# Kernel tuning notes

Hardware: AMD Instinct MI355X
Metric: run time of the kernel (lower is better)

The kernel has to match this reference:

```python
import jax, jax.numpy as jnp
import numpy as np
from jax import lax

CIN, COUT, K, PAD = 256, 128, 3, 1


def setup_inputs() -> dict:
    key = jax.random.key(0)
    ks = jax.random.split(key, 5)
    N, h0, w0 = 2, 64, 64
    x = jax.random.normal(ks[0], (N, CIN, h0, w0), jnp.float32)
    lateral_feat = jax.random.normal(ks[1], (N, COUT, 1, 1), jnp.float32)
    trans_w = jax.random.normal(ks[2], (CIN, COUT, K, K), jnp.float32) * 0.02
    off_w1 = jax.random.normal(ks[3], (64, COUT, 3, 3), jnp.float32) * 0.02
    off_b1 = jnp.zeros((64,), jnp.float32)
    off_w2 = jax.random.normal(ks[4], (2 * K * K, 64, 3, 3), jnp.float32) * 0.02
    off_b2 = jnp.zeros((2 * K * K,), jnp.float32)
    return dict(x=x, lateral_feat=lateral_feat, trans_w=trans_w,
                off_w1=off_w1, off_b1=off_b1, off_w2=off_w2, off_b2=off_b2)


def _conv2d(x, w, b, pad):
    y = lax.conv_general_dilated(x, w, (1, 1), [(pad, pad), (pad, pad)],
                                 dimension_numbers=('NCHW', 'OIHW', 'NCHW'))
    return y + b[None, :, None, None]


def _conv_transpose2d(x, w, stride, pad, out_pad):
    # torch ConvTranspose2d weight layout: [Cin, Cout, k, k]
    k = w.shape[2]
    wt = jnp.flip(w, (2, 3)).transpose(1, 0, 2, 3)  # [Cout, Cin, k, k]
    lo = k - 1 - pad
    hi = k - 1 - pad + out_pad
    return lax.conv_general_dilated(x, wt, (1, 1), [(lo, hi), (lo, hi)],
                                    lhs_dilation=(stride, stride),
                                    dimension_numbers=('NCHW', 'OIHW', 'NCHW'))


def _deform_conv2d(x, offset, w, pad):
    # x [N,C,H,W], offset [N,2*K*K,H,W] (y,x interleaved per kernel tap), w [O,C,K,K]
    N, C, H, W = x.shape
    O = w.shape[0]
    KK = K * K
    off = offset.reshape(N, KK, 2, H, W)
    ky = jnp.arange(KK) // K
    kx = jnp.arange(KK) % K
    py = jnp.arange(H)[None, None, :, None] + (ky - pad)[None, :, None, None] + off[:, :, 0]
    px = jnp.arange(W)[None, None, None, :] + (kx - pad)[None, :, None, None] + off[:, :, 1]
    y0 = jnp.floor(py)
    x0 = jnp.floor(px)
    dy = py - y0
    dx = px - x0
    y0i = y0.astype(jnp.int32)
    x0i = x0.astype(jnp.int32)
    xf = x.reshape(N, C, H * W)

    def corner(yi, xi, wgt):
        valid = (yi >= 0) & (yi < H) & (xi >= 0) & (xi < W)
        idx = (jnp.clip(yi, 0, H - 1) * W + jnp.clip(xi, 0, W - 1)).reshape(N, -1)
        v = jnp.take_along_axis(xf, idx[:, None, :], axis=2).reshape(N, C, KK, H, W)
        return v * (wgt * valid)[:, None]

    sampled = (corner(y0i, x0i, (1 - dy) * (1 - dx))
               + corner(y0i, x0i + 1, (1 - dy) * dx)
               + corner(y0i + 1, x0i, dy * (1 - dx))
               + corner(y0i + 1, x0i + 1, dy * dx))  # [N,C,KK,H,W]
    return jnp.einsum('nckhw,ock->nohw', sampled, w.reshape(O, C, KK))


def reference(x, lateral_feat, trans_w, off_w1, off_b1, off_w2, off_b2):
    up = _conv_transpose2d(x, trans_w, 2, PAD, 1)          # [N, COUT, 2h0, 2w0]
    h = jax.nn.relu(_conv2d(lateral_feat, off_w1, off_b1, 1))
    offset = jnp.tanh(_conv2d(h, off_w2, off_b2, 1))       # [N, 18, 1, 1]
    N, C, H, W = up.shape
    # offset.repeat(1, 1, H, W) with 1x1 spatial input == broadcast to full grid
    offset = jnp.broadcast_to(offset, (N, 2 * K * K, H, W))
    # deform_conv2d uses trans_conv weight [O=CIN, I=COUT, K, K], stride=1, pad=PAD
    return _deform_conv2d(up, offset, trans_w, PAD)        # [N, CIN, H, W]
```

## Files before the change

### kernel.cpp

```cpp
#include <hip/hip_runtime.h>
#include <hip/hip_fp16.h>
#include <math.h>

typedef __attribute__((ext_vector_type(8))) _Float16 f16x8;
typedef __attribute__((ext_vector_type(4))) float f32x4;

__device__ __forceinline__ unsigned short f2h(float f) {
    __half h = __float2half_rn(f);
    union { __half h; unsigned short u; } v; v.h = h; return v.u;
}
__device__ __forceinline__ unsigned pk2h(float lo, float hi) {
    __half2 h = __floats2half2_rn(lo, hi);
    union { __half2 h; unsigned u; } v; v.h = h; return v.u;
}

#define BARRIER() do { asm volatile("s_waitcnt lgkmcnt(0)" ::: "memory"); \
                       __builtin_amdgcn_s_barrier(); } while (0)

__device__ __forceinline__ void blend_store_h(uint4 uA, uint4 uB, uint4 uC, uint4 uD,
                                              __half2 w0, __half2 w1, __half2 w2, __half2 w3,
                                              unsigned short* dst) {
    union U { uint4 u; __half2 h[4]; };
    U a, b, c, d, r;
    a.u = uA; b.u = uB; c.u = uC; d.u = uD;
#pragma unroll
    for (int i = 0; i < 4; ++i)
        r.h[i] = __hfma2(w0, a.h[i], __hfma2(w1, b.h[i], __hfma2(w2, c.h[i], __hmul2(w3, d.h[i]))));
    *(uint4*)dst = r.u;
}

__global__ __launch_bounds__(256) void k_prep(const float* __restrict__ x,
                                              const float* __restrict__ lat,
                                              const float* __restrict__ tw,
                                              const float* __restrict__ w1,
                                              const float* __restrict__ b1,
                                              const float* __restrict__ w2,
                                              const float* __restrict__ b2,
                                              unsigned short* __restrict__ xp,
                                              unsigned short* __restrict__ A2f,
                                              unsigned short* __restrict__ Awf,
                                              unsigned short* __restrict__ upp,
                                              int* __restrict__ ipar,
                                              float* __restrict__ fpar) {
    __shared__ float sm[8420];
    int b = blockIdx.x, t = threadIdx.x;
    if (b == 0) {
        for (int i = t; i < 8192; i += 256) sm[(i >> 7) * 129 + (i & 127)] = w1[i * 9 + 4];
        __syncthreads();
        if (t < 128) {
            int n = t >> 6, o = t & 63;
            float s = b1[o];
            const float* ln = lat + n * 128;
#pragma unroll 8
            for (int c = 0; c < 128; ++c) s += ln[c] * sm[o * 129 + c];
            sm[8256 + t] = fmaxf(s, 0.f);
        }
        __syncthreads();
        if (t < 36) {
            int n = t / 18, j = t % 18;
            float s = b2[j];
            for (int o = 0; o < 64; ++o) s += sm[8256 + n * 64 + o] * w2[(j * 64 + o) * 9 + 4];
            float ov = tanhf(s);
            ov = fminf(fmaxf(ov, -0.999999f), 0.999999f);
            sm[8384 + t] = ov;
        }
        __syncthreads();
        if (t < 36) {
            int n = t / 18, j = t % 18;
            int tap = j >> 1, d = j & 1;
            float ov = sm[8384 + t];
            float fl = floorf(ov);
            int kc = d ? (tap % 3) : (tap / 3);
            ipar[(n * 9 + tap) * 2 + d] = kc - 1 + (int)fl;
            fpar[(n * 9 + tap) * 2 + d] = ov - fl;
        }
    } else if (b < 145) {
        int slot = (b - 1) * 256 + t;
        int l = slot & 63;
        int mi = (slot >> 6) & 3;
        int w = (slot >> 8) & 3;
        int k = slot >> 10;
        int row = w * 64 + mi * 16 + (l & 15);
        int kq = l >> 4;
        unsigned short v[8];
#pragma unroll
        for (int j = 0; j < 8; ++j) {
            int kcol = k * 32 + kq * 8 + j;
            int tap = kcol >> 7, c = kcol & 127;
            v[j] = f2h(tw[(row * 128 + c) * 9 + tap]);
        }
        unsigned p0 = (unsigned)v[0] | ((unsigned)v[1] << 16);
        unsigned p1 = (unsigned)v[2] | ((unsigned)v[3] << 16);
        unsigned p2 = (unsigned)v[4] | ((unsigned)v[5] << 16);
        unsigned p3 = (unsigned)v[6] | ((unsigned)v[7] << 16);
        *(uint4*)(A2f + slot * 8) = make_uint4(p0, p1, p2, p3);
    } else if (b < 289) {
        int slot = (b - 145) * 256 + t;
        int l = slot & 63;
        int mi = (slot >> 6) & 3;
        int wm = (slot >> 8) & 1;
        int k = slot >> 9;
        int row = wm * 64 + mi * 16 + (l & 15);
        int kq = l >> 4;
        unsigned short v[8];
#pragma unroll
        for (int j = 0; j < 8; ++j) {
            int kcol = k * 32 + kq * 8 + j;
            int t9 = kcol >> 8, ci = kcol & 255;
            int ky = t9 / 3, kx = t9 - ky * 3;
            v[j] = f2h(tw[(ci * 128 + row) * 9 + (2 - ky) * 3 + (2 - kx)]);
        }
        unsigned p0 = (unsigned)v[0] | ((unsigned)v[1] << 16);
        unsigned p1 = (unsigned)v[2] | ((unsigned)v[3] << 16);
        unsigned p2 = (unsigned)v[4] | ((unsigned)v[5] << 16);
        unsigned p3 = (unsigned)v[6] | ((unsigned)v[7] << 16);
        *(uint4*)(Awf + slot * 8) = make_uint4(p0, p1, p2, p3);
    } else if (b < 801) {
        int bb = b - 289;
        int h = bb & 63, cq = (bb >> 6) & 3, n = bb >> 8;
        int c0 = cq * 64;
        {
            int wcol = t & 63, sub = t >> 6;
            for (int r = 0; r < 16; ++r) {
                int ci_l = r * 4 + sub;
                sm[ci_l * 65 + wcol] = x[((n * 256 + c0 + ci_l) * 64 + h) * 64 + wcol];
            }
        }
        __syncthreads();
        int wcol = t >> 2, cg = t & 3;
        unsigned short* dst = xp + (size_t)n * (65 * 65 * 256) + (h * 65 + wcol) * 256 + c0 + cg * 16;
        unsigned pk[8];
#pragma unroll
        for (int j = 0; j < 8; ++j)
            pk[j] = pk2h(sm[(cg * 16 + 2 * j) * 65 + wcol], sm[(cg * 16 + 2 * j + 1) * 65 + wcol]);
        *(uint4*)dst = make_uint4(pk[0], pk[1], pk[2], pk[3]);
        *(uint4*)(dst + 8) = make_uint4(pk[4], pk[5], pk[6], pk[7]);
    } else {
        int g = (b - 801) * 256 + t;
        int n2 = g >= 16640 ? 1 : 0;
        int i = g - n2 * 16640;
        int px_id = i >> 4, chv = i & 15;
        int r, c;
        if (px_id < 528) {
            int rr = px_id / 132;
            r = rr < 2 ? rr : 128 + rr;
            c = px_id - rr * 132;
        } else {
            int jj = px_id - 528;
            r = 2 + (jj >> 2);
            int cc = jj & 3;
            c = cc < 2 ? cc : 128 + cc;
        }
        uint4* p = (uint4*)(upp + (size_t)n2 * (132 * 132 * 128) + ((r * 132 + c) * 128) + chv * 8);
        *p = make_uint4(0u, 0u, 0u, 0u);
    }
}

__global__ __launch_bounds__(256) void k_tconv3(const unsigned short* __restrict__ xp,
                                                const unsigned short* __restrict__ Awf,
                                                unsigned short* __restrict__ upp) {
    __shared__ unsigned short Bs[2][2][64][40];
    __shared__ int st9[4];
    __shared__ int sbb[4];
    int t = threadIdx.x;
    int b = blockIdx.x;
    int phase = b & 1;
    int xpar = ((b >> 1) & 1) ^ phase;
    int n = (b >> 2) & 1;
    int yh = b >> 3;
    int y = yh * 2 + phase;
    const unsigned short* xpn = xp + (size_t)n * (65 * 65 * 256);

    int lane = t & 63, w = t >> 6;
    int col = lane & 15, q = lane >> 4;
    int wm = w >> 1, wn = w & 1;
    int bx = t >> 2, bcg = t & 3;
    int boff = bx * 256 + bcg * 8;

    int kys[2], kxs[2], nky, nkx;
    if (phase) { kys[0] = 0; kys[1] = 2; nky = 2; } else { kys[0] = 1; kys[1] = 1; nky = 1; }
    if (xpar)  { kxs[0] = 0; kxs[1] = 2; nkx = 2; } else { kxs[0] = 1; kxs[1] = 1; nkx = 1; }
    int nslots = nky * nkx;
    if (t < 4) {
        int tc = t < nslots ? t : 0;
        int a1 = (nkx == 2) ? (tc >> 1) : tc;
        int a2 = (nkx == 2) ? (tc & 1) : 0;
        int ky = kys[a1], kx = kxs[a2];
        st9[t] = ky * 3 + kx;
        int d2 = (y + ky - 1) >> 1;
        int s = (xpar + kx - 1) >> 1;
        sbb[t] = (d2 * 65 + s) * 256;
    }
    int NPAIR = nslots * 4;

    f32x4 acc[4][2];
#pragma unroll
    for (int mi = 0; mi < 4; ++mi)
#pragma unroll
        for (int ni = 0; ni < 2; ++ni) acc[mi][ni] = (f32x4){0.f, 0.f, 0.f, 0.f};

    __syncthreads();

    const unsigned short* Afw = Awf + wm * 2048 + lane * 8;
    f16x8 aC[2][4], aN[2][4];
    uint4 nb0, nb1;

    {
        const unsigned short* pT = xpn + sbb[0] + boff;
        uint4 b0 = *(const uint4*)pT;
        uint4 b1 = *(const uint4*)(pT + 32);
        const unsigned short* ap = Afw + st9[0] * 32768;
#pragma unroll
        for (int mi = 0; mi < 4; ++mi) {
            aC[0][mi] = *(const f16x8*)(ap + mi * 512);
            aC[1][mi] = *(const f16x8*)(ap + 4096 + mi * 512);
        }
        *(uint4*)&Bs[0][0][bx][bcg * 8] = b0;
        *(uint4*)&Bs[0][1][bx][bcg * 8] = b1;
    }
    BARRIER();

#define TC_PH(PP, BUF, AC, AN)                                                   \
    {                                                                            \
        int P_ = (PP);                                                           \
        if (P_ + 1 < NPAIR) {                                                    \
            int slot_ = (P_ + 1) >> 2;                                           \
            int cb0_ = ((P_ + 1) & 3) * 2;                                       \
            const unsigned short* pT_ = xpn + sbb[slot_] + cb0_ * 32 + boff;     \
            nb0 = *(const uint4*)pT_;                                            \
            nb1 = *(const uint4*)(pT_ + 32);                                     \
            const unsigned short* ap_ = Afw + (st9[slot_] * 8 + cb0_) * 4096;    \
            _Pragma("unroll")                                                    \
            for (int mi = 0; mi < 4; ++mi) {                                     \
                AN[0][mi] = *(const f16x8*)(ap_ + mi * 512);                     \
                AN[1][mi] = *(const f16x8*)(ap_ + 4096 + mi * 512);              \
            }                                                                    \
        }                                                                        \
        f16x8 bb[2][2];                                                          \
        _Pragma("unroll")                                                        \
        for (int c = 0; c < 2; ++c)                                              \
            _Pragma("unroll")                                                    \
            for (int ni = 0; ni < 2; ++ni)                                       \
                bb[c][ni] = *(const f16x8*)&Bs[BUF][c][wn * 32 + ni * 16 + col][q * 8]; \
        __builtin_amdgcn_s_setprio(1);                                           \
        _Pragma("unroll")                                                        \
        for (int c = 0; c < 2; ++c)                                              \
            _Pragma("unroll")                                                    \
            for (int mi = 0; mi < 4; ++mi)                                       \
                _Pragma("unroll")                                                \
                for (int ni = 0; ni < 2; ++ni)                                   \
                    acc[mi][ni] = __builtin_amdgcn_mfma_f32_16x16x32_f16(AC[c][mi], bb[c][ni], acc[mi][ni], 0, 0, 0); \
        __builtin_amdgcn_s_setprio(0);                                           \
        if (P_ + 1 < NPAIR) {                                                    \
            *(uint4*)&Bs[BUF ^ 1][0][bx][bcg * 8] = nb0;                         \
            *(uint4*)&Bs[BUF ^ 1][1][bx][bcg * 8] = nb1;                         \
        }                                                                        \
        BARRIER();                                                               \
    }

    for (int pp = 0; pp < NPAIR; pp += 2) {
        TC_PH(pp,     0, aC, aN);
        TC_PH(pp + 1, 1, aN, aC);
    }
#undef TC_PH

    unsigned short* uppn = upp + (size_t)n * (132 * 132 * 128);
#pragma unroll
    for (int mi = 0; mi < 4; ++mi)
#pragma unroll
        for (int ni = 0; ni < 2; ++ni) {
            int co = wm * 64 + mi * 16 + q * 4;
            int p64 = wn * 32 + ni * 16 + col;
            int xg = 2 * p64 + xpar;
            unsigned short* p = uppn + ((y + 2) * 132 + (xg + 2)) * 128 + co;
            unsigned lo = pk2h(acc[mi][ni][0], acc[mi][ni][1]);
            unsigned hi = pk2h(acc[mi][ni][2], acc[mi][ni][3]);
            *(uint2*)p = make_uint2(lo, hi);
        }
}

__global__ __launch_bounds__(256) void k_deform3(const unsigned short* __restrict__ upp,
                                                 const unsigned short* __restrict__ A2f,
                                                 const int* __restrict__ ipar,
                                                 const float* __restrict__ fpar,
                                                 float* __restrict__ out) {
    __shared__ unsigned short Bs[2][2][64][40];
    __shared__ int sbase[9];
    __shared__ __half2 swh[9][4];
    int t = threadIdx.x;
    int b = blockIdx.x;
    int xcd = b & 7, j = b >> 3;
    int n = xcd >> 2, band = xcd & 3;
    int y = band * 32 + (j & 31);
    int tx0 = (j >> 5) * 64;
    const unsigned short* uppn = upp + (size_t)n * (132 * 132 * 128);

    int lane = t & 63, w = t >> 6;
    int col = lane & 15, q = lane >> 4;
    int bx = t >> 2, bcg = t & 3;
    int boff = bx * 128 + bcg * 8;

    if (t < 9) {
        int iy = ipar[(n * 9 + t) * 2 + 0], ix = ipar[(n * 9 + t) * 2 + 1];
        float fy = fpar[(n * 9 + t) * 2 + 0], fx = fpar[(n * 9 + t) * 2 + 1];
        sbase[t] = ((y + 2 + iy) * 132 + (tx0 + 2 + ix)) * 128;
        swh[t][0] = __float2half2_rn((1.f - fy) * (1.f - fx));
        swh[t][1] = __float2half2_rn((1.f - fy) * fx);
        swh[t][2] = __float2half2_rn(fy * (1.f - fx));
        swh[t][3] = __float2half2_rn(fy * fx);
    }

    f32x4 acc[4][4];
#pragma unroll
    for (int mi = 0; mi < 4; ++mi)
#pragma unroll
        for (int ni = 0; ni < 4; ++ni) acc[mi][ni] = (f32x4){0.f, 0.f, 0.f, 0.f};

    __syncthreads();

    const unsigned short* Afw = A2f + w * 2048 + lane * 8;
    f16x8 aC[2][4], aN[2][4];
    uint4 cA0, cB0, cC0, cD0, cA1, cB1, cC1, cD1;

    {
        const unsigned short* pAt = uppn + sbase[0] + boff;
        const unsigned short* pCt = pAt + 16896;
        __half2 w0 = swh[0][0], w1 = swh[0][1], w2 = swh[0][2], w3 = swh[0][3];
        uint4 uA0 = *(const uint4*)pAt;
        uint4 uB0 = *(const uint4*)(pAt + 128);
        uint4 uC0 = *(const uint4*)pCt;
        uint4 uD0 = *(const uint4*)(pCt + 128);
        uint4 uA1 = *(const uint4*)(pAt + 32);
        uint4 uB1 = *(const uint4*)(pAt + 160);
        uint4 uC1 = *(const uint4*)(pCt + 32);
        uint4 uD1 = *(const uint4*)(pCt + 160);
#pragma unroll
        for (int mi = 0; mi < 4; ++mi) {
            aC[0][mi] = *(const f16x8*)(Afw + mi * 512);
            aC[1][mi] = *(const f16x8*)(Afw + 8192 + mi * 512);
        }
        blend_store_h(uA0, uB0, uC0, uD0, w0, w1, w2, w3, &Bs[0][0][bx][bcg * 8]);
        blend_store_h(uA1, uB1, uC1, uD1, w0, w1, w2, w3, &Bs[0][1][bx][bcg * 8]);
    }
    BARRIER();

#define DEF_PH(PP, BUF, AC, AN)                                                  \
    {                                                                            \
        int P_ = (PP);                                                           \
        __half2 w0_, w1_, w2_, w3_;                                              \
        if (P_ + 1 < 18) {                                                       \
            int tap_ = (P_ + 1) >> 1;                                            \
            int sh_ = ((P_ + 1) & 1) * 64;                                       \
            int sb_ = sbase[tap_];                                               \
            w0_ = swh[tap_][0]; w1_ = swh[tap_][1];                              \
            w2_ = swh[tap_][2]; w3_ = swh[tap_][3];                              \
            const unsigned short* pAt_ = uppn + sb_ + boff + sh_;                \
            const unsigned short* pCt_ = pAt_ + 16896;                           \
            cA0 = *(const uint4*)pAt_;                                           \
            cB0 = *(const uint4*)(pAt_ + 128);                                   \
            cC0 = *(const uint4*)pCt_;                                           \
            cD0 = *(const uint4*)(pCt_ + 128);                                   \
            cA1 = *(const uint4*)(pAt_ + 32);                                    \
            cB1 = *(const uint4*)(pAt_ + 160);                                   \
            cC1 = *(const uint4*)(pCt_ + 32);                                    \
            cD1 = *(const uint4*)(pCt_ + 160);                                   \
            const unsigned short* ap_ = Afw + (P_ + 1) * 16384;                  \
            _Pragma("unroll")                                                    \
            for (int mi = 0; mi < 4; ++mi) {                                     \
                AN[0][mi] = *(const f16x8*)(ap_ + mi * 512);                     \
                AN[1][mi] = *(const f16x8*)(ap_ + 8192 + mi * 512);              \
            }                                                                    \
        }                                                                        \
        f16x8 bb[2][4];                                                          \
        _Pragma("unroll")                                                        \
        for (int c = 0; c < 2; ++c)                                              \
            _Pragma("unroll")                                                    \
            for (int ni = 0; ni < 4; ++ni)                                       \
                bb[c][ni] = *(const f16x8*)&Bs[BUF][c][ni * 16 + col][q * 8];    \
        __builtin_amdgcn_s_setprio(1);                                           \
        _Pragma("unroll")                                                        \
        for (int c = 0; c < 2; ++c)                                              \
            _Pragma("unroll")                                                    \
            for (int mi = 0; mi < 4; ++mi)                                       \
                _Pragma("unroll")                                                \
                for (int ni = 0; ni < 4; ++ni)                                   \
                    acc[mi][ni] = __builtin_amdgcn_mfma_f32_16x16x32_f16(AC[c][mi], bb[c][ni], acc[mi][ni], 0, 0, 0); \
        __builtin_amdgcn_s_setprio(0);                                           \
        if (P_ + 1 < 18) {                                                       \
            blend_store_h(cA0, cB0, cC0, cD0, w0_, w1_, w2_, w3_, &Bs[BUF ^ 1][0][bx][bcg * 8]); \
            blend_store_h(cA1, cB1, cC1, cD1, w0_, w1_, w2_, w3_, &Bs[BUF ^ 1][1][bx][bcg * 8]); \
        }                                                                        \
        BARRIER();                                                               \
    }

    for (int pp = 0; pp < 18; pp += 2) {
        DEF_PH(pp,     0, aC, aN);
        DEF_PH(pp + 1, 1, aN, aC);
    }
#undef DEF_PH

#pragma unroll
    for (int mi = 0; mi < 4; ++mi)
#pragma unroll
        for (int ni = 0; ni < 4; ++ni) {
            int o = w * 64 + mi * 16 + q * 4;
            int xg = tx0 + ni * 16 + col;
            float* p = out + (((size_t)(n * 256 + o)) * 128 + y) * 128 + xg;
            p[0]         = acc[mi][ni][0];
            p[16384]     = acc[mi][ni][1];
            p[2 * 16384] = acc[mi][ni][2];
            p[3 * 16384] = acc[mi][ni][3];
        }
}

extern "C" void kernel_launch(void* const* d_in, const int* in_sizes, int n_in,
                              void* d_out, int out_size, void* d_ws, size_t ws_size,
                              hipStream_t stream) {
    const float* x   = (const float*)d_in[0];
    const float* lat = (const float*)d_in[1];
    const float* tw  = (const float*)d_in[2];
    const float* w1  = (const float*)d_in[3];
    const float* b1  = (const float*)d_in[4];
    const float* w2  = (const float*)d_in[5];
    const float* b2  = (const float*)d_in[6];
    float* out = (float*)d_out;

    char* ws = (char*)d_ws;
    unsigned short* upp = (unsigned short*)ws;
    unsigned short* xp  = (unsigned short*)(ws + 8921088);
    unsigned short* A2f = (unsigned short*)(ws + 13247488);
    unsigned short* Awf = (unsigned short*)(ws + 13837312);
    int*   ipar         = (int*)(ws + 14427136);
    float* fpar         = (float*)(ws + 14427424);

    hipMemsetAsync(ws + 8921088, 0, 4326400, stream);
    k_prep<<<931, 256, 0, stream>>>(x, lat, tw, w1, b1, w2, b2, xp, A2f, Awf, upp, ipar, fpar);
    k_tconv3<<<512, 256, 0, stream>>>(xp, Awf, upp);
    k_deform3<<<512, 256, 0, stream>>>(upp, A2f, ipar, fpar, out);
}
```

Measured before the change: 147.0 us.

## Stage upsampled input window in LDS and reorder deform loop by channel half

The deform kernel now cooperatively loads a 5-row by 68-pixel window of the upsampled feature map into shared memory for each 64-channel half. It then performs the bilinear blends for all nine taps from LDS instead of issuing per-tap global loads, reordering the K loop from tap-major to channel-half-major. This cuts redundant global and L2 traffic across the overlapping taps, at the cost of roughly 43KB more LDS per block and an extra barrier per half, which may lower occupancy. The s_setprio hints around the MFMA blocks are also dropped in both kernels.

```diff
diff --git a/kernel.cpp b/kernel.cpp
--- a/kernel.cpp
+++ b/kernel.cpp
@@ -242,7 +242,6 @@
             _Pragma("unroll")                                                    \
             for (int ni = 0; ni < 2; ++ni)                                       \
                 bb[c][ni] = *(const f16x8*)&Bs[BUF][c][wn * 32 + ni * 16 + col][q * 8]; \
-        __builtin_amdgcn_s_setprio(1);                                           \
         _Pragma("unroll")                                                        \
         for (int c = 0; c < 2; ++c)                                              \
             _Pragma("unroll")                                                    \
@@ -250,7 +249,6 @@
                 _Pragma("unroll")                                                \
                 for (int ni = 0; ni < 2; ++ni)                                   \
                     acc[mi][ni] = __builtin_amdgcn_mfma_f32_16x16x32_f16(AC[c][mi], bb[c][ni], acc[mi][ni], 0, 0, 0); \
-        __builtin_amdgcn_s_setprio(0);                                           \
         if (P_ + 1 < NPAIR) {                                                    \
             *(uint4*)&Bs[BUF ^ 1][0][bx][bcg * 8] = nb0;                         \
             *(uint4*)&Bs[BUF ^ 1][1][bx][bcg * 8] = nb1;                         \
@@ -279,13 +277,14 @@
         }
 }
 
-__global__ __launch_bounds__(256) void k_deform3(const unsigned short* __restrict__ upp,
+__global__ __launch_bounds__(256) void k_deform4(const unsigned short* __restrict__ upp,
                                                  const unsigned short* __restrict__ A2f,
                                                  const int* __restrict__ ipar,
                                                  const float* __restrict__ fpar,
                                                  float* __restrict__ out) {
+    __shared__ unsigned short Ws[2][5][68][32];
     __shared__ unsigned short Bs[2][2][64][40];
-    __shared__ int sbase[9];
+    __shared__ int sR0[9], sDx[9];
     __shared__ __half2 swh[9][4];
     int t = threadIdx.x;
     int b = blockIdx.x;
@@ -298,12 +297,12 @@
     int lane = t & 63, w = t >> 6;
     int col = lane & 15, q = lane >> 4;
     int bx = t >> 2, bcg = t & 3;
-    int boff = bx * 128 + bcg * 8;
 
     if (t < 9) {
         int iy = ipar[(n * 9 + t) * 2 + 0], ix = ipar[(n * 9 + t) * 2 + 1];
         float fy = fpar[(n * 9 + t) * 2 + 0], fx = fpar[(n * 9 + t) * 2 + 1];
-        sbase[t] = ((y + 2 + iy) * 132 + (tx0 + 2 + ix)) * 128;
+        sR0[t] = iy + 2;
+        sDx[t] = ix + 2;
         swh[t][0] = __float2half2_rn((1.f - fy) * (1.f - fx));
         swh[t][1] = __float2half2_rn((1.f - fy) * fx);
         swh[t][2] = __float2half2_rn(fy * (1.f - fx));
@@ -320,51 +319,23 @@
 
     const unsigned short* Afw = A2f + w * 2048 + lane * 8;
     f16x8 aC[2][4], aN[2][4];
-    uint4 cA0, cB0, cC0, cD0, cA1, cB1, cC1, cD1;
-
-    {
-        const unsigned short* pAt = uppn + sbase[0] + boff;
-        const unsigned short* pCt = pAt + 16896;
-        __half2 w0 = swh[0][0], w1 = swh[0][1], w2 = swh[0][2], w3 = swh[0][3];
-        uint4 uA0 = *(const uint4*)pAt;
-        uint4 uB0 = *(const uint4*)(pAt + 128);
-        uint4 uC0 = *(const uint4*)pCt;
-        uint4 uD0 = *(const uint4*)(pCt + 128);
-        uint4 uA1 = *(const uint4*)(pAt + 32);
-        uint4 uB1 = *(const uint4*)(pAt + 160);
-        uint4 uC1 = *(const uint4*)(pCt + 32);
-        uint4 uD1 = *(const uint4*)(pCt + 160);
-#pragma unroll
-        for (int mi = 0; mi < 4; ++mi) {
-            aC[0][mi] = *(const f16x8*)(Afw + mi * 512);
-            aC[1][mi] = *(const f16x8*)(Afw + 8192 + mi * 512);
-        }
-        blend_store_h(uA0, uB0, uC0, uD0, w0, w1, w2, w3, &Bs[0][0][bx][bcg * 8]);
-        blend_store_h(uA1, uB1, uC1, uD1, w0, w1, w2, w3, &Bs[0][1][bx][bcg * 8]);
-    }
-    BARRIER();
-
-#define DEF_PH(PP, BUF, AC, AN)                                                  \
+
+#define BLEND_WS(CHUNK, TAP, DST)                                                \
     {                                                                            \
-        int P_ = (PP);                                                           \
-        __half2 w0_, w1_, w2_, w3_;                                              \
-        if (P_ + 1 < 18) {                                                       \
-            int tap_ = (P_ + 1) >> 1;                                            \
-            int sh_ = ((P_ + 1) & 1) * 64;                                       \
-            int sb_ = sbase[tap_];                                               \
-            w0_ = swh[tap_][0]; w1_ = swh[tap_][1];                              \
-            w2_ = swh[tap_][2]; w3_ = swh[tap_][3];                              \
-            const unsigned short* pAt_ = uppn + sb_ + boff + sh_;                \
-            const unsigned short* pCt_ = pAt_ + 16896;                           \
-            cA0 = *(const uint4*)pAt_;                                           \
-            cB0 = *(const uint4*)(pAt_ + 128);                                   \
-            cC0 = *(const uint4*)pCt_;                                           \
-            cD0 = *(const uint4*)(pCt_ + 128);                                   \
-            cA1 = *(const uint4*)(pAt_ + 32);                                    \
-            cB1 = *(const uint4*)(pAt_ + 160);                                   \
-            cC1 = *(const uint4*)(pCt_ + 32);                                    \
-            cD1 = *(const uint4*)(pCt_ + 160);                                   \
-            const unsigned short* ap_ = Afw + (P_ + 1) * 16384;                  \
+        int r0_ = sR0[TAP], dx_ = sDx[TAP];                                      \
+        const unsigned short* pA_ = &Ws[CHUNK][0][0][0] + (r0_ * 68 + bx + dx_) * 32 + bcg * 8; \
+        uint4 uA_ = *(const uint4*)pA_;                                          \
+        uint4 uB_ = *(const uint4*)(pA_ + 32);                                   \
+        uint4 uC_ = *(const uint4*)(pA_ + 68 * 32);                              \
+        uint4 uD_ = *(const uint4*)(pA_ + 68 * 32 + 32);                         \
+        blend_store_h(uA_, uB_, uC_, uD_, swh[TAP][0], swh[TAP][1],              \
+                      swh[TAP][2], swh[TAP][3], DST);                            \
+    }
+
+#define DEF_TAU(TAU, BUF, AC, AN, S)                                             \
+    {                                                                            \
+        if ((TAU) < 8) {                                                         \
+            const unsigned short* ap_ = Afw + (((TAU) + 1) * 4 + (S) * 2) * 8192;\
             _Pragma("unroll")                                                    \
             for (int mi = 0; mi < 4; ++mi) {                                     \
                 AN[0][mi] = *(const f16x8*)(ap_ + mi * 512);                     \
@@ -377,7 +348,6 @@
             _Pragma("unroll")                                                    \
             for (int ni = 0; ni < 4; ++ni)                                       \
                 bb[c][ni] = *(const f16x8*)&Bs[BUF][c][ni * 16 + col][q * 8];    \
-        __builtin_amdgcn_s_setprio(1);                                           \
         _Pragma("unroll")                                                        \
         for (int c = 0; c < 2; ++c)                                              \
             _Pragma("unroll")                                                    \
@@ -385,19 +355,47 @@
                 _Pragma("unroll")                                                \
                 for (int ni = 0; ni < 4; ++ni)                                   \
                     acc[mi][ni] = __builtin_amdgcn_mfma_f32_16x16x32_f16(AC[c][mi], bb[c][ni], acc[mi][ni], 0, 0, 0); \
-        __builtin_amdgcn_s_setprio(0);                                           \
-        if (P_ + 1 < 18) {                                                       \
-            blend_store_h(cA0, cB0, cC0, cD0, w0_, w1_, w2_, w3_, &Bs[BUF ^ 1][0][bx][bcg * 8]); \
-            blend_store_h(cA1, cB1, cC1, cD1, w0_, w1_, w2_, w3_, &Bs[BUF ^ 1][1][bx][bcg * 8]); \
+        if ((TAU) < 8) {                                                         \
+            BLEND_WS(0, (TAU) + 1, &Bs[BUF ^ 1][0][bx][bcg * 8]);                \
+            BLEND_WS(1, (TAU) + 1, &Bs[BUF ^ 1][1][bx][bcg * 8]);                \
         }                                                                        \
         BARRIER();                                                               \
     }
 
-    for (int pp = 0; pp < 18; pp += 2) {
-        DEF_PH(pp,     0, aC, aN);
-        DEF_PH(pp + 1, 1, aN, aC);
-    }
-#undef DEF_PH
+    for (int s = 0; s < 2; ++s) {
+        for (int i = t; i < 2720; i += 256) {
+            int c2 = i / 1360;
+            int rem2 = i - c2 * 1360;
+            int row = rem2 / 272;
+            int rem = rem2 - row * 272;
+            int px = rem >> 2, cg4 = rem & 3;
+            uint4 v = *(const uint4*)&uppn[(size_t)((y + row) * 132 + tx0 + px) * 128 + s * 64 + c2 * 32 + cg4 * 8];
+            *(uint4*)(&Ws[c2][0][0][0] + (row * 68 + px) * 32 + cg4 * 8) = v;
+        }
+        BARRIER();
+        {
+            const unsigned short* ap0 = Afw + s * 16384;
+#pragma unroll
+            for (int mi = 0; mi < 4; ++mi) {
+                aC[0][mi] = *(const f16x8*)(ap0 + mi * 512);
+                aC[1][mi] = *(const f16x8*)(ap0 + 8192 + mi * 512);
+            }
+            BLEND_WS(0, 0, &Bs[0][0][bx][bcg * 8]);
+            BLEND_WS(1, 0, &Bs[0][1][bx][bcg * 8]);
+        }
+        BARRIER();
+        DEF_TAU(0, 0, aC, aN, s);
+        DEF_TAU(1, 1, aN, aC, s);
+        DEF_TAU(2, 0, aC, aN, s);
+        DEF_TAU(3, 1, aN, aC, s);
+        DEF_TAU(4, 0, aC, aN, s);
+        DEF_TAU(5, 1, aN, aC, s);
+        DEF_TAU(6, 0, aC, aN, s);
+        DEF_TAU(7, 1, aN, aC, s);
+        DEF_TAU(8, 0, aC, aN, s);
+    }
+#undef DEF_TAU
+#undef BLEND_WS
 
 #pragma unroll
     for (int mi = 0; mi < 4; ++mi)
@@ -436,5 +434,5 @@
     hipMemsetAsync(ws + 8921088, 0, 4326400, stream);
     k_prep<<<931, 256, 0, stream>>>(x, lat, tw, w1, b1, w2, b2, xp, A2f, Awf, upp, ipar, fpar);
     k_tconv3<<<512, 256, 0, stream>>>(xp, Awf, upp);
-    k_deform3<<<512, 256, 0, stream>>>(upp, A2f, ipar, fpar, out);
-}
+    k_deform4<<<512, 256, 0, stream>>>(upp, A2f, ipar, fpar, out);
+}
```

Result: faster. 131.2 us (-10.7%).
